# Optimization experiments

Measured on AMD Instinct MI355X. Metric: run time of the kernel, lower is better.

## Reference

```python
import jax, jax.numpy as jnp
import numpy as np

N_GAUSS = 4096
M_POINTS = 65536
EPS = 1e-6


def setup_inputs() -> dict:
    key = jax.random.key(0)
    k1, k2, k3, k4, k5 = jax.random.split(key, 5)
    sample_points = jax.random.uniform(k1, (M_POINTS, 3), dtype=jnp.float32)
    positions = jax.random.uniform(k2, (N_GAUSS, 3), dtype=jnp.float32)
    # realistic Gaussian widths around initial_scale = 0.1 / N^(1/3)
    scales = 0.05 + 0.10 * jax.random.uniform(k3, (N_GAUSS, 3), dtype=jnp.float32)
    rotations = jax.random.normal(k4, (N_GAUSS, 4), dtype=jnp.float32)
    intensities = 0.5 * jax.random.uniform(k5, (N_GAUSS,), dtype=jnp.float32)
    return {
        "sample_points": sample_points,
        "positions": positions,
        "scales": scales,
        "rotations": rotations,
        "intensities": intensities,
    }


def _quat_to_rotmat(quats):
    # quats: (N,4) -> (N,3,3), matches torch module's normalization (+1e-8)
    q = quats / (jnp.linalg.norm(quats, axis=1, keepdims=True) + 1e-8)
    w, x, y, z = q[:, 0], q[:, 1], q[:, 2], q[:, 3]
    R = jnp.stack([
        jnp.stack([1 - 2 * (y * y + z * z), 2 * (x * y - z * w), 2 * (x * z + y * w)], axis=-1),
        jnp.stack([2 * (x * y + z * w), 1 - 2 * (x * x + z * z), 2 * (y * z - x * w)], axis=-1),
        jnp.stack([2 * (x * z - y * w), 2 * (y * z + x * w), 1 - 2 * (x * x + y * y)], axis=-1),
    ], axis=-2)
    return R  # (N,3,3)


def reference(sample_points, positions, scales, rotations, intensities):
    # f(x_m) = sum_n w_n * exp(-0.5 * (x_m - mu_n)^T A_n (x_m - mu_n)),
    # A_n = R_n diag(1/s_n^2) R_n^T  (inverse covariance)
    s = jnp.abs(scales) + EPS                              # (N,3)
    R = _quat_to_rotmat(rotations)                         # (N,3,3)
    inv_s2 = 1.0 / (s * s)                                 # (N,3)
    A = jnp.einsum('nij,nj,nkj->nik', R, inv_s2, R)        # (N,3,3)
    b = jnp.einsum('nij,nj->ni', A, positions)             # (N,3)
    c = jnp.einsum('ni,ni->n', b, positions)               # (N,)
    M = sample_points.shape[0]
    X2 = (sample_points[:, :, None] * sample_points[:, None, :]).reshape(M, 9)  # (M,9)
    Aflat = A.reshape(-1, 9)                               # (N,9)
    # (M,N) Mahalanobis distances via two GEMMs (no (M,N,3) intermediate)
    q = X2 @ Aflat.T - 2.0 * (sample_points @ b.T) + c[None, :]
    out = jnp.exp(-0.5 * q) @ intensities                  # (M,)
    return out
```

## Files before the change

kernel.cpp:

```cpp
#include <hip/hip_runtime.h>


#define M_POINTS 65536
#define N_GAUSS  4096
#define KNEG     (-0.72134752044448170f)

typedef _Float16 half8  __attribute__((ext_vector_type(8)));
typedef float    float4v __attribute__((ext_vector_type(4)));

__device__ __forceinline__ float fast_exp2(float x) {
#if defined(__has_builtin)
#if __has_builtin(__builtin_amdgcn_exp2f)
    return __builtin_amdgcn_exp2f(x);
#else
    return exp2f(x);
#endif
#else
    return exp2f(x);
#endif
}

__global__ __launch_bounds__(64) void precompute_bfrag(
    const float* __restrict__ pos, const float* __restrict__ scl,
    const float* __restrict__ rot, const float* __restrict__ inten,
    half8* __restrict__ bfrag)
{
    int n = blockIdx.x * 64 + threadIdx.x;
    if (n >= N_GAUSS) return;

    float qw = rot[4*n+0], qx = rot[4*n+1], qy = rot[4*n+2], qz = rot[4*n+3];
    float nrm = sqrtf(qw*qw + qx*qx + qy*qy + qz*qz) + 1e-8f;
    float ir = 1.0f / nrm;
    qw *= ir; qx *= ir; qy *= ir; qz *= ir;

    float r00 = 1.f - 2.f*(qy*qy + qz*qz);
    float r01 = 2.f*(qx*qy - qz*qw);
    float r02 = 2.f*(qx*qz + qy*qw);
    float r10 = 2.f*(qx*qy + qz*qw);
    float r11 = 1.f - 2.f*(qx*qx + qz*qz);
    float r12 = 2.f*(qy*qz - qx*qw);
    float r20 = 2.f*(qx*qz - qy*qw);
    float r21 = 2.f*(qy*qz + qx*qw);
    float r22 = 1.f - 2.f*(qx*qx + qy*qy);

    float s0 = fabsf(scl[3*n+0]) + 1e-6f;
    float s1 = fabsf(scl[3*n+1]) + 1e-6f;
    float s2 = fabsf(scl[3*n+2]) + 1e-6f;
    float w0 = 1.f/(s0*s0), w1 = 1.f/(s1*s1), w2 = 1.f/(s2*s2);

    float a00 = r00*r00*w0 + r01*r01*w1 + r02*r02*w2;
    float a01 = r00*r10*w0 + r01*r11*w1 + r02*r12*w2;
    float a02 = r00*r20*w0 + r01*r21*w1 + r02*r22*w2;
    float a11 = r10*r10*w0 + r11*r11*w1 + r12*r12*w2;
    float a12 = r10*r20*w0 + r11*r21*w1 + r12*r22*w2;
    float a22 = r20*r20*w0 + r21*r21*w1 + r22*r22*w2;

    float p0 = pos[3*n+0], p1 = pos[3*n+1], p2 = pos[3*n+2];
    float b0 = a00*p0 + a01*p1 + a02*p2;
    float b1 = a01*p0 + a11*p1 + a12*p2;
    float b2 = a02*p0 + a12*p1 + a22*p2;
    float c  = b0*p0 + b1*p1 + b2*p2;

    float I = fmaxf(inten[n], 1e-30f);

    float C[10];
    C[0] = KNEG * a00;       C[1] = KNEG * a11;       C[2] = KNEG * a22;
    C[3] = 2.f*KNEG * a01;   C[4] = 2.f*KNEG * a02;   C[5] = 2.f*KNEG * a12;
    C[6] = -2.f*KNEG * b0;   C[7] = -2.f*KNEG * b1;   C[8] = -2.f*KNEG * b2;
    C[9] = KNEG * c + log2f(I);

    _Float16 chi[10], clo[10];
#pragma unroll
    for (int j = 0; j < 10; ++j) {
        chi[j] = (_Float16)C[j];
        clo[j] = (_Float16)(C[j] - (float)chi[j]);
    }

    const int tile = n >> 4, nl = n & 15;
#pragma unroll
    for (int q = 0; q < 4; ++q) {
        half8 v;
#pragma unroll
        for (int j = 0; j < 8; ++j) {
            const int k = q*8 + j;
            _Float16 h = (_Float16)0.f;
            if (k < 30) {
                const int jm = k / 3, s = k % 3;
                h = (s == 2) ? clo[jm] : chi[jm];
            }
            v[j] = h;
        }
        bfrag[tile*64 + q*16 + nl] = v;
    }
}

__global__ __launch_bounds__(256) void gauss_eval(
    const float* __restrict__ pts,
    const half8* __restrict__ bfrag,
    float* __restrict__ out)
{
    __shared__ half8 lds[2 * 16 * 64];

    const int tid  = threadIdx.x;
    const int lane = tid & 63;
    const int wv   = tid >> 6;
    const int ml   = lane & 15;
    const int q    = lane >> 4;

    const int ptbase = blockIdx.x * 64 + wv * 16;
    const int pt = ptbase + ml;
    const float x = pts[3*pt+0], y = pts[3*pt+1], z = pts[3*pt+2];
    const float P[10] = {x*x, y*y, z*z, x*y, x*z, y*z, x, y, z, 1.f};

    _Float16 v[32];
#pragma unroll
    for (int j = 0; j < 10; ++j) {
        _Float16 hi = (_Float16)P[j];
        _Float16 lo = (_Float16)(P[j] - (float)hi);
        v[3*j]   = hi;
        v[3*j+1] = lo;
        v[3*j+2] = hi;
    }
    v[30] = (_Float16)0.f; v[31] = (_Float16)0.f;

    half8 afrag;
#pragma unroll
    for (int j = 0; j < 8; ++j) {
        _Float16 lo01 = (q & 1) ? v[8 + j]  : v[j];
        _Float16 hi23 = (q & 1) ? v[24 + j] : v[16 + j];
        afrag[j] = (q & 2) ? hi23 : lo01;
    }

    float acc0 = 0.f, acc1 = 0.f, acc2 = 0.f, acc3 = 0.f;
    const float4v zero4 = {0.f, 0.f, 0.f, 0.f};

    {
        const half8* src = bfrag + (0 + wv*4) * 64;
        half8* dst = lds + (wv*4) * 64;
#pragma unroll
        for (int i = 0; i < 4; ++i) dst[i*64 + lane] = src[i*64 + lane];
    }
    __syncthreads();

    for (int r = 0; r < 16; ++r) {
        const half8* cur = lds + (r & 1) * 1024;
        half8* nxt       = lds + ((r + 1) & 1) * 1024;

        if (r < 15) {
            const half8* src = bfrag + ((r+1)*16 + wv*4) * 64;
            half8* dst = nxt + (wv*4) * 64;
#pragma unroll
            for (int i = 0; i < 4; ++i) dst[i*64 + lane] = src[i*64 + lane];
        }

#pragma unroll
        for (int i = 0; i < 16; ++i) {
            half8 b = cur[i*64 + lane];
            float4v d = __builtin_amdgcn_mfma_f32_16x16x32_f16(afrag, b, zero4, 0, 0, 0);
            acc0 += fast_exp2(d[0]);
            acc1 += fast_exp2(d[1]);
            acc2 += fast_exp2(d[2]);
            acc3 += fast_exp2(d[3]);
        }
        __syncthreads();
    }

#pragma unroll
    for (int m = 1; m <= 8; m <<= 1) {
        acc0 += __shfl_xor(acc0, m);
        acc1 += __shfl_xor(acc1, m);
        acc2 += __shfl_xor(acc2, m);
        acc3 += __shfl_xor(acc3, m);
    }

    if (ml == 0) {
        float4 o;
        o.x = acc0; o.y = acc1; o.z = acc2; o.w = acc3;
        *(float4*)(out + ptbase + q*4) = o;
    }
}

extern "C" void kernel_launch(void* const* d_in, const int* in_sizes, int n_in,
                              void* d_out, int out_size, void* d_ws, size_t ws_size,
                              hipStream_t stream) {
    const float* sample_points = (const float*)d_in[0];
    const float* positions     = (const float*)d_in[1];
    const float* scales        = (const float*)d_in[2];
    const float* rotations     = (const float*)d_in[3];
    const float* intensities   = (const float*)d_in[4];

    half8* bfrag = (half8*)d_ws;

    precompute_bfrag<<<N_GAUSS / 64, 64, 0, stream>>>(
        positions, scales, rotations, intensities, bfrag);

    gauss_eval<<<M_POINTS / 64, 256, 0, stream>>>(
        sample_points, bfrag, (float*)d_out);
}
```

Measured before the change: 110.3 us.

## Register-block four point fragments per wave and split Gaussians across blocks with atomics

Each wave now holds four A fragments (64 points) and reuses every B fragment loaded from LDS across four MFMAs, cutting LDS traffic per MFMA by four. The Gaussian dimension is split across four grid rows, so each block covers a quarter of the tiles, and partial sums are combined with atomicAdd into an output that the precompute kernel now zeroes. This trades more registers, lower occupancy and atomic traffic for better data reuse while keeping the grid at 1024 blocks.

New measurement: 198.4 us. 1.8x slower.

```diff
diff --git a/kernel.cpp b/kernel.cpp
--- a/kernel.cpp
+++ b/kernel.cpp
@@ -5,7 +5,7 @@
 #define N_GAUSS  4096
 #define KNEG     (-0.72134752044448170f)
 
-typedef _Float16 half8  __attribute__((ext_vector_type(8)));
+typedef _Float16 half8   __attribute__((ext_vector_type(8)));
 typedef float    float4v __attribute__((ext_vector_type(4)));
 
 __device__ __forceinline__ float fast_exp2(float x) {
@@ -20,13 +20,21 @@
 #endif
 }
 
-__global__ __launch_bounds__(64) void precompute_bfrag(
+__global__ __launch_bounds__(256) void precompute_bfrag(
     const float* __restrict__ pos, const float* __restrict__ scl,
     const float* __restrict__ rot, const float* __restrict__ inten,
-    half8* __restrict__ bfrag)
+    half8* __restrict__ bfrag, float4* __restrict__ out_zero)
 {
-    int n = blockIdx.x * 64 + threadIdx.x;
+    int n = blockIdx.x * 256 + threadIdx.x;
     if (n >= N_GAUSS) return;
+
+    {
+        float4 z = make_float4(0.f, 0.f, 0.f, 0.f);
+        out_zero[n]         = z;
+        out_zero[n + 4096]  = z;
+        out_zero[n + 8192]  = z;
+        out_zero[n + 12288] = z;
+    }
 
     float qw = rot[4*n+0], qx = rot[4*n+1], qy = rot[4*n+2], qz = rot[4*n+3];
     float nrm = sqrtf(qw*qw + qx*qx + qy*qy + qz*qz) + 1e-8f;
@@ -94,12 +102,18 @@
     }
 }
 
-__global__ __launch_bounds__(256) void gauss_eval(
+#define PT_SLABS  256
+#define G_SPLIT   4
+#define G_TILES   (256 / G_SPLIT)
+#define RT        16
+#define ROUNDS    (G_TILES / RT)
+
+__global__ __launch_bounds__(256, 4) void gauss_eval(
     const float* __restrict__ pts,
     const half8* __restrict__ bfrag,
     float* __restrict__ out)
 {
-    __shared__ half8 lds[2 * 16 * 64];
+    __shared__ half8 lds[2 * RT * 64];
 
     const int tid  = threadIdx.x;
     const int lane = tid & 63;
@@ -107,76 +121,94 @@
     const int ml   = lane & 15;
     const int q    = lane >> 4;
 
-    const int ptbase = blockIdx.x * 64 + wv * 16;
-    const int pt = ptbase + ml;
-    const float x = pts[3*pt+0], y = pts[3*pt+1], z = pts[3*pt+2];
-    const float P[10] = {x*x, y*y, z*z, x*y, x*z, y*z, x, y, z, 1.f};
-
-    _Float16 v[32];
-#pragma unroll
-    for (int j = 0; j < 10; ++j) {
-        _Float16 hi = (_Float16)P[j];
-        _Float16 lo = (_Float16)(P[j] - (float)hi);
-        v[3*j]   = hi;
-        v[3*j+1] = lo;
-        v[3*j+2] = hi;
-    }
-    v[30] = (_Float16)0.f; v[31] = (_Float16)0.f;
-
-    half8 afrag;
-#pragma unroll
-    for (int j = 0; j < 8; ++j) {
-        _Float16 lo01 = (q & 1) ? v[8 + j]  : v[j];
-        _Float16 hi23 = (q & 1) ? v[24 + j] : v[16 + j];
-        afrag[j] = (q & 2) ? hi23 : lo01;
-    }
-
-    float acc0 = 0.f, acc1 = 0.f, acc2 = 0.f, acc3 = 0.f;
+    const int base = blockIdx.x * 256 + wv * 64;
+    half8 af[4];
+#pragma unroll
+    for (int f = 0; f < 4; ++f) {
+        const int pt = base + f*16 + ml;
+        const float x = pts[3*pt+0], y = pts[3*pt+1], z = pts[3*pt+2];
+        const float P[10] = {x*x, y*y, z*z, x*y, x*z, y*z, x, y, z, 1.f};
+        _Float16 v[32];
+#pragma unroll
+        for (int j = 0; j < 10; ++j) {
+            _Float16 hi = (_Float16)P[j];
+            _Float16 lo = (_Float16)(P[j] - (float)hi);
+            v[3*j]   = hi;
+            v[3*j+1] = lo;
+            v[3*j+2] = hi;
+        }
+        v[30] = (_Float16)0.f; v[31] = (_Float16)0.f;
+#pragma unroll
+        for (int j = 0; j < 8; ++j) {
+            _Float16 lo01 = (q & 1) ? v[8 + j]  : v[j];
+            _Float16 hi23 = (q & 1) ? v[24 + j] : v[16 + j];
+            af[f][j] = (q & 2) ? hi23 : lo01;
+        }
+    }
+
+    float acc[4][4];
+#pragma unroll
+    for (int f = 0; f < 4; ++f)
+#pragma unroll
+        for (int r = 0; r < 4; ++r) acc[f][r] = 0.f;
     const float4v zero4 = {0.f, 0.f, 0.f, 0.f};
 
+    const int gtile0 = blockIdx.y * G_TILES;
+
     {
-        const half8* src = bfrag + (0 + wv*4) * 64;
+        const half8* src = bfrag + (gtile0 + wv*4) * 64;
         half8* dst = lds + (wv*4) * 64;
 #pragma unroll
         for (int i = 0; i < 4; ++i) dst[i*64 + lane] = src[i*64 + lane];
     }
     __syncthreads();
 
-    for (int r = 0; r < 16; ++r) {
-        const half8* cur = lds + (r & 1) * 1024;
-        half8* nxt       = lds + ((r + 1) & 1) * 1024;
-
-        if (r < 15) {
-            const half8* src = bfrag + ((r+1)*16 + wv*4) * 64;
+    for (int r = 0; r < ROUNDS; ++r) {
+        const half8* cur = lds + (r & 1) * (RT*64);
+        half8* nxt       = lds + ((r + 1) & 1) * (RT*64);
+
+        if (r < ROUNDS - 1) {
+            const half8* src = bfrag + (gtile0 + (r+1)*RT + wv*4) * 64;
             half8* dst = nxt + (wv*4) * 64;
 #pragma unroll
             for (int i = 0; i < 4; ++i) dst[i*64 + lane] = src[i*64 + lane];
         }
 
 #pragma unroll
-        for (int i = 0; i < 16; ++i) {
+        for (int i = 0; i < RT; ++i) {
             half8 b = cur[i*64 + lane];
-            float4v d = __builtin_amdgcn_mfma_f32_16x16x32_f16(afrag, b, zero4, 0, 0, 0);
-            acc0 += fast_exp2(d[0]);
-            acc1 += fast_exp2(d[1]);
-            acc2 += fast_exp2(d[2]);
-            acc3 += fast_exp2(d[3]);
+            float4v d0 = __builtin_amdgcn_mfma_f32_16x16x32_f16(af[0], b, zero4, 0, 0, 0);
+            float4v d1 = __builtin_amdgcn_mfma_f32_16x16x32_f16(af[1], b, zero4, 0, 0, 0);
+            float4v d2 = __builtin_amdgcn_mfma_f32_16x16x32_f16(af[2], b, zero4, 0, 0, 0);
+            float4v d3 = __builtin_amdgcn_mfma_f32_16x16x32_f16(af[3], b, zero4, 0, 0, 0);
+#pragma unroll
+            for (int r4 = 0; r4 < 4; ++r4) {
+                acc[0][r4] += fast_exp2(d0[r4]);
+                acc[1][r4] += fast_exp2(d1[r4]);
+                acc[2][r4] += fast_exp2(d2[r4]);
+                acc[3][r4] += fast_exp2(d3[r4]);
+            }
         }
         __syncthreads();
     }
 
 #pragma unroll
     for (int m = 1; m <= 8; m <<= 1) {
-        acc0 += __shfl_xor(acc0, m);
-        acc1 += __shfl_xor(acc1, m);
-        acc2 += __shfl_xor(acc2, m);
-        acc3 += __shfl_xor(acc3, m);
+#pragma unroll
+        for (int f = 0; f < 4; ++f) {
+#pragma unroll
+            for (int r = 0; r < 4; ++r)
+                acc[f][r] += __shfl_xor(acc[f][r], m);
+        }
     }
 
     if (ml == 0) {
-        float4 o;
-        o.x = acc0; o.y = acc1; o.z = acc2; o.w = acc3;
-        *(float4*)(out + ptbase + q*4) = o;
+#pragma unroll
+        for (int f = 0; f < 4; ++f) {
+#pragma unroll
+            for (int r = 0; r < 4; ++r)
+                atomicAdd(&out[base + f*16 + q*4 + r], acc[f][r]);
+        }
     }
 }
 
@@ -191,9 +223,9 @@
 
     half8* bfrag = (half8*)d_ws;
 
-    precompute_bfrag<<<N_GAUSS / 64, 64, 0, stream>>>(
-        positions, scales, rotations, intensities, bfrag);
-
-    gauss_eval<<<M_POINTS / 64, 256, 0, stream>>>(
+    precompute_bfrag<<<N_GAUSS / 256, 256, 0, stream>>>(
+        positions, scales, rotations, intensities, bfrag, (float4*)d_out);
+
+    gauss_eval<<<dim3(PT_SLABS, G_SPLIT), 256, 0, stream>>>(
         sample_points, bfrag, (float*)d_out);
 }
```
